# Optimization experiments

Measured on AMD Instinct MI355X. Metric: run time of the kernel, lower is better.

Reference implementation:

```python
import jax, jax.numpy as jnp
import numpy as np

N_NODES, N_EDGES, F_IN, H1, H2, N_CLASSES = 10000, 640000, 128, 64, 32, 16


def gcn_conv(x, W, b, src, dst, n_nodes):
    """PyG GCNConv: x' = D^{-1/2} (A + I) D^{-1/2} (x W) + b, deg from dst + self-loop."""
    h = x @ W  # [N, out]
    deg = jax.ops.segment_sum(jnp.ones(src.shape[0], h.dtype), dst,
                              num_segments=n_nodes) + 1.0  # +1 self-loop
    dinv = jax.lax.rsqrt(deg)  # [N]
    coef = dinv[src] * dinv[dst]  # [E]
    agg = jax.ops.segment_sum(h[src] * coef[:, None], dst, num_segments=n_nodes)
    agg = agg + h * (dinv * dinv)[:, None]  # self-loop contribution
    return agg + b


def setup_inputs() -> dict:
    key = jax.random.key(0)
    ks = jax.random.split(key, 8)
    x = jax.random.normal(ks[0], (N_NODES, F_IN), jnp.float32)
    edge_index = jax.random.randint(ks[1], (2, N_EDGES), 0, N_NODES, jnp.int32)
    W1 = jax.random.normal(ks[2], (F_IN, H1), jnp.float32) / np.sqrt(F_IN)
    b1 = jnp.zeros((H1,), jnp.float32)
    W2 = jax.random.normal(ks[3], (H1, H2), jnp.float32) / np.sqrt(H1)
    b2 = jnp.zeros((H2,), jnp.float32)
    Wfc = jax.random.normal(ks[4], (H2, N_CLASSES), jnp.float32) / np.sqrt(H2)
    bfc = jnp.zeros((N_CLASSES,), jnp.float32)
    return {"x": x, "W1": W1, "b1": b1, "W2": W2, "b2": b2,
            "Wfc": Wfc, "bfc": bfc, "edge_index": edge_index}


def reference(x, W1, b1, W2, b2, Wfc, bfc, edge_index):
    src, dst = edge_index[0], edge_index[1]
    n = x.shape[0]
    h = jax.nn.relu(gcn_conv(x, W1, b1, src, dst, n))
    # dropout p=0.5 is identity in eval mode
    h = jax.nn.relu(gcn_conv(h, W2, b2, src, dst, n))
    g = jnp.mean(h, axis=0)  # [H2]
    return g @ Wfc + bfc  # [num_classes]
```

## Files before the change

kernel.cpp:

```cpp
#include <hip/hip_runtime.h>
#include <hip/hip_bf16.h>

#define N_NODES 10000
#define N_EDGES 640000
#define F_IN 128
#define H1 64
#define H2 32
#define N_CLASSES 16

#define NB 128
#define NPB 79
#define STAGE_C 64
#define SLOT 6144
#define IDX_CAP 4096
#define PART_BLOCKS 313

typedef unsigned short ushortT;

__device__ __forceinline__ float bf_lo(unsigned u) {
    u <<= 16; float f; __builtin_memcpy(&f, &u, 4); return f;
}
__device__ __forceinline__ float bf_hi(unsigned u) {
    u &= 0xffff0000u; float f; __builtin_memcpy(&f, &u, 4); return f;
}
__device__ __forceinline__ unsigned bf_pack(float a, float b) {
    __hip_bfloat16 ha = __float2bfloat16(a), hb = __float2bfloat16(b);
    unsigned short ua, ub;
    __builtin_memcpy(&ua, &ha, 2); __builtin_memcpy(&ub, &hb, 2);
    return (unsigned)ua | ((unsigned)ub << 16);
}

__global__ void __launch_bounds__(256) k_part_gemm1(const int* __restrict__ src,
                                                    const int* __restrict__ dst,
                                                    int* __restrict__ bucketCursor,
                                                    int* __restrict__ partBuf,
                                                    const float* __restrict__ x,
                                                    const float* __restrict__ W1,
                                                    float* __restrict__ h1f,
                                                    const float* __restrict__ bfc,
                                                    float* __restrict__ out) {
    __shared__ __align__(16) char pool[40960];
    int t = threadIdx.x;
    if (blockIdx.x < PART_BLOCKS) {
        int* cnt   = (int*)pool;
        int* gbase = (int*)(pool + 512);
        int* stage = (int*)(pool + 1024);
        if (t < NB) cnt[t] = 0;
        __syncthreads();
        const int4* src4 = (const int4*)src;
        const int4* dst4 = (const int4*)dst;
#pragma unroll
        for (int k = 0; k < 2; ++k) {
            int i4 = blockIdx.x * 512 + k * 256 + t;
            if (i4 < N_EDGES / 4) {
                int4 s = src4[i4];
                int4 d = dst4[i4];
                int b, l, p;
                b = d.x / NPB; l = d.x - b * NPB; p = atomicAdd(&cnt[b], 1); stage[b * STAGE_C + p] = s.x | (l << 14);
                b = d.y / NPB; l = d.y - b * NPB; p = atomicAdd(&cnt[b], 1); stage[b * STAGE_C + p] = s.y | (l << 14);
                b = d.z / NPB; l = d.z - b * NPB; p = atomicAdd(&cnt[b], 1); stage[b * STAGE_C + p] = s.z | (l << 14);
                b = d.w / NPB; l = d.w - b * NPB; p = atomicAdd(&cnt[b], 1); stage[b * STAGE_C + p] = s.w | (l << 14);
            }
        }
        __syncthreads();
        if (t < NB) gbase[t] = atomicAdd(&bucketCursor[t], cnt[t]);
        __syncthreads();
        for (int i = t; i < NB * STAGE_C; i += 256) {
            int b = i >> 6;
            int k = i & (STAGE_C - 1);
            if (k < cnt[b]) partBuf[b * SLOT + gbase[b] + k] = stage[i];
        }
    } else {
        int gb = blockIdx.x - PART_BLOCKS;
        float* w1s = (float*)pool;
        float* xs  = (float*)(pool + 32768);
        int node0 = gb * 16;
        const float4* W14 = (const float4*)W1;
        float4* w1s4 = (float4*)w1s;
#pragma unroll
        for (int i = 0; i < 8; ++i) w1s4[i * 256 + t] = W14[i * 256 + t];
        const float4* x4 = (const float4*)(x + (long)node0 * F_IN);
        float4* xs4 = (float4*)xs;
#pragma unroll
        for (int i = 0; i < 2; ++i) xs4[i * 256 + t] = x4[i * 256 + t];
        if (gb == 0 && t < N_CLASSES) out[t] = bfc[t];
        __syncthreads();
        int j = t & 63;
        int q = t >> 6;
        int r0 = q * 4;
        float acc0 = 0.f, acc1 = 0.f, acc2 = 0.f, acc3 = 0.f;
#pragma unroll 4
        for (int k = 0; k < F_IN; ++k) {
            float w = w1s[k * H1 + j];
            acc0 += xs[(r0 + 0) * F_IN + k] * w;
            acc1 += xs[(r0 + 1) * F_IN + k] * w;
            acc2 += xs[(r0 + 2) * F_IN + k] * w;
            acc3 += xs[(r0 + 3) * F_IN + k] * w;
        }
        int v0 = node0 + r0;
        h1f[(v0 + 0) * H1 + j] = acc0;
        h1f[(v0 + 1) * H1 + j] = acc1;
        h1f[(v0 + 2) * H1 + j] = acc2;
        h1f[(v0 + 3) * H1 + j] = acc3;
    }
}

__global__ void __launch_bounds__(512) k_bsort(const int* __restrict__ bucketCursor,
                                               const int* __restrict__ partBuf,
                                               ushortT* __restrict__ srcU,
                                               int* __restrict__ rowStart,
                                               float* __restrict__ dinv,
                                               const float* __restrict__ h1f,
                                               __hip_bfloat16* __restrict__ h1b) {
    __shared__ int sc[NB];
    __shared__ int ldeg[NPB];
    __shared__ int lpre[NPB];
    __shared__ int cur[NPB];
    __shared__ float sdv[NPB];
    int t = threadIdx.x;
    int b = blockIdx.x;
    if (b == 0 && t == 0) rowStart[N_NODES] = N_EDGES;
    if (t < NB) sc[t] = bucketCursor[t];
    __syncthreads();
    for (int off = 1; off < NB; off <<= 1) {
        int v = (t >= off && t < NB) ? sc[t - off] : 0;
        __syncthreads();
        if (t < NB) sc[t] += v;
        __syncthreads();
    }
    int cnt = bucketCursor[b];
    int base = sc[b] - cnt;
    int nodeBase = b * NPB;
    int nNodes = N_NODES - nodeBase;
    if (nNodes <= 0) return;
    if (nNodes > NPB) nNodes = NPB;
    if (t < NPB) ldeg[t] = 0;
    __syncthreads();
    for (int i = t; i < cnt; i += 512) {
        int p = partBuf[b * SLOT + i];
        atomicAdd(&ldeg[p >> 14], 1);
    }
    __syncthreads();
    if (t == 0) {
        int run = 0;
        for (int i = 0; i < nNodes; ++i) { lpre[i] = run; run += ldeg[i]; }
    }
    __syncthreads();
    if (t < nNodes) {
        int v = nodeBase + t;
        rowStart[v] = base + lpre[t];
        cur[t] = lpre[t];
        float dv_ = rsqrtf((float)ldeg[t] + 1.0f);
        dinv[v] = dv_;
        sdv[t] = dv_;
    }
    __syncthreads();
    for (int i = t; i < cnt; i += 512) {
        int p = partBuf[b * SLOT + i];
        int pos = atomicAdd(&cur[p >> 14], 1);
        srcU[base + pos] = (ushortT)(p & 16383);
    }
    unsigned* h1u = (unsigned*)h1b;
    for (int i = t; i < nNodes * 32; i += 512) {
        int ln = i >> 5, p = i & 31;
        int v = nodeBase + ln;
        float2 f2 = ((const float2*)(h1f + v * H1))[p];
        float d = sdv[ln];
        h1u[v * 32 + p] = bf_pack(f2.x * d, f2.y * d);
    }
}

__global__ void __launch_bounds__(256) k_gather1_gemm2(const __hip_bfloat16* __restrict__ h1b,
                                const int* __restrict__ rowStart,
                                const ushortT* __restrict__ srcU,
                                const float* __restrict__ dinv,
                                const float* __restrict__ b1,
                                const float* __restrict__ W2,
                                __hip_bfloat16* __restrict__ h2b) {
    __shared__ float h1s[8][H1];
    __shared__ ushortT idxs[IDX_CAP];
    __shared__ int sRange[2];
    int t = threadIdx.x;
    int n  = t >> 5;
    int fp = t & 31;
    int v = blockIdx.x * 8 + n;
    if (t == 0) { sRange[0] = rowStart[blockIdx.x * 8]; sRange[1] = rowStart[blockIdx.x * 8 + 8]; }
    __syncthreads();
    int rs0 = sRange[0];
    int cnt0 = sRange[1] - rs0;
    bool useLds = (cnt0 <= IDX_CAP);
    if (useLds) for (int i = t; i < cnt0; i += 256) idxs[i] = srcU[rs0 + i];
    float dv_ = dinv[v];
    int rs = rowStart[v], re = rowStart[v + 1];
    const unsigned* h1u = (const unsigned*)h1b;
    unsigned su = h1u[v * 32 + fp];
    float fx = bf_lo(su), fy = bf_hi(su);
    float x0 = 0.f, y0 = 0.f, x1 = 0.f, y1 = 0.f;
    float x2 = 0.f, y2 = 0.f, x3 = 0.f, y3 = 0.f;
    __syncthreads();
    if (useLds) {
        int le = rs - rs0, lend = re - rs0;
        for (; le + 4 <= lend; le += 4) {
            int i0 = idxs[le],     i1 = idxs[le + 1];
            int i2 = idxs[le + 2], i3 = idxs[le + 3];
            unsigned u0 = h1u[i0 * 32 + fp];
            unsigned u1 = h1u[i1 * 32 + fp];
            unsigned u2 = h1u[i2 * 32 + fp];
            unsigned u3 = h1u[i3 * 32 + fp];
            x0 += bf_lo(u0); y0 += bf_hi(u0);
            x1 += bf_lo(u1); y1 += bf_hi(u1);
            x2 += bf_lo(u2); y2 += bf_hi(u2);
            x3 += bf_lo(u3); y3 += bf_hi(u3);
        }
        for (; le < lend; ++le) {
            unsigned u = h1u[idxs[le] * 32 + fp];
            fx += bf_lo(u); fy += bf_hi(u);
        }
    } else {
        for (int e = rs; e < re; ++e) {
            unsigned u = h1u[(int)srcU[e] * 32 + fp];
            fx += bf_lo(u); fy += bf_hi(u);
        }
    }
    fx += (x0 + x1) + (x2 + x3);
    fy += (y0 + y1) + (y2 + y3);
    ((float2*)h1s[n])[fp] = make_float2(fmaxf(dv_ * fx + b1[fp * 2], 0.f),
                                        fmaxf(dv_ * fy + b1[fp * 2 + 1], 0.f));
    __syncthreads();
    float acc = 0.f;
#pragma unroll
    for (int kk = 0; kk < H1; ++kk)
        acc += h1s[n][kk] * W2[kk * H2 + fp];
    h2b[v * H2 + fp] = __float2bfloat16(acc * dv_);
}

__global__ void __launch_bounds__(256) k_gather2_out(const __hip_bfloat16* __restrict__ h2b,
                               const int* __restrict__ rowStart,
                               const ushortT* __restrict__ srcU,
                               const float* __restrict__ dinv,
                               const float* __restrict__ b2,
                               const float* __restrict__ Wfc,
                               float* __restrict__ out) {
    __shared__ float red[16][H2];
    __shared__ ushortT idxs[IDX_CAP];
    __shared__ int sRange[2];
    __shared__ float gs[H2];
    int t = threadIdx.x;
    int n  = t >> 4;
    int fp = t & 15;
    int v = blockIdx.x * 16 + n;
    if (t == 0) { sRange[0] = rowStart[blockIdx.x * 16]; sRange[1] = rowStart[blockIdx.x * 16 + 16]; }
    __syncthreads();
    int rs0 = sRange[0];
    int cnt0 = sRange[1] - rs0;
    bool useLds = (cnt0 <= IDX_CAP);
    if (useLds) for (int i = t; i < cnt0; i += 256) idxs[i] = srcU[rs0 + i];
    float dv_ = dinv[v];
    int rs = rowStart[v], re = rowStart[v + 1];
    const unsigned* h2u = (const unsigned*)h2b;
    unsigned su = h2u[v * 16 + fp];
    float fx = bf_lo(su), fy = bf_hi(su);
    float x0 = 0.f, y0 = 0.f, x1 = 0.f, y1 = 0.f;
    float x2 = 0.f, y2 = 0.f, x3 = 0.f, y3 = 0.f;
    __syncthreads();
    if (useLds) {
        int le = rs - rs0, lend = re - rs0;
        for (; le + 4 <= lend; le += 4) {
            int i0 = idxs[le],     i1 = idxs[le + 1];
            int i2 = idxs[le + 2], i3 = idxs[le + 3];
            unsigned u0 = h2u[i0 * 16 + fp];
            unsigned u1 = h2u[i1 * 16 + fp];
            unsigned u2 = h2u[i2 * 16 + fp];
            unsigned u3 = h2u[i3 * 16 + fp];
            x0 += bf_lo(u0); y0 += bf_hi(u0);
            x1 += bf_lo(u1); y1 += bf_hi(u1);
            x2 += bf_lo(u2); y2 += bf_hi(u2);
            x3 += bf_lo(u3); y3 += bf_hi(u3);
        }
        for (; le < lend; ++le) {
            unsigned u = h2u[idxs[le] * 16 + fp];
            fx += bf_lo(u); fy += bf_hi(u);
        }
    } else {
        for (int e = rs; e < re; ++e) {
            unsigned u = h2u[(int)srcU[e] * 16 + fp];
            fx += bf_lo(u); fy += bf_hi(u);
        }
    }
    fx += (x0 + x1) + (x2 + x3);
    fy += (y0 + y1) + (y2 + y3);
    ((float2*)red[n])[fp] = make_float2(fmaxf(dv_ * fx + b2[fp * 2], 0.f),
                                        fmaxf(dv_ * fy + b2[fp * 2 + 1], 0.f));
    __syncthreads();
    if (t < H2) {
        float s = 0.f;
#pragma unroll
        for (int r = 0; r < 16; ++r) s += red[r][t];
        gs[t] = s;
    }
    __syncthreads();
    if (t < N_CLASSES) {
        float acc = 0.f;
#pragma unroll
        for (int j = 0; j < H2; ++j)
            acc += gs[j] * Wfc[j * N_CLASSES + t];
        atomicAdd(&out[t], acc * (1.0f / (float)N_NODES));
    }
}

extern "C" void kernel_launch(void* const* d_in, const int* in_sizes, int n_in,
                              void* d_out, int out_size, void* d_ws, size_t ws_size,
                              hipStream_t stream) {
    const float* x   = (const float*)d_in[0];
    const float* W1  = (const float*)d_in[1];
    const float* b1  = (const float*)d_in[2];
    const float* W2  = (const float*)d_in[3];
    const float* b2  = (const float*)d_in[4];
    const float* Wfc = (const float*)d_in[5];
    const float* bfc = (const float*)d_in[6];
    const int* edge = (const int*)d_in[7];
    const int* srcI = edge;
    const int* dstI = edge + N_EDGES;
    float* out = (float*)d_out;

    char* ws = (char*)d_ws;
    int*     bucketCursor = (int*)    (ws + 0);
    float*   dinv         = (float*)  (ws + 1024);
    int*     rowStart     = (int*)    (ws + 41984);
    ushortT* srcU         = (ushortT*)(ws + 82944);
    int*     partBuf      = (int*)    (ws + 1363968);
    float*   h1f          = (float*)  (ws + 4509696);
    __hip_bfloat16* h1b   = (__hip_bfloat16*)(ws + 7069696);
    __hip_bfloat16* h2b   = (__hip_bfloat16*)(ws + 8349696);

    hipMemsetAsync(bucketCursor, 0, 512, stream);

    k_part_gemm1<<<PART_BLOCKS + N_NODES / 16, 256, 0, stream>>>(
        srcI, dstI, bucketCursor, partBuf, x, W1, h1f, bfc, out);
    k_bsort<<<NB, 512, 0, stream>>>(bucketCursor, partBuf, srcU, rowStart, dinv,
                                    h1f, h1b);
    k_gather1_gemm2<<<N_NODES / 8, 256, 0, stream>>>(h1b, rowStart, srcU,
                                                     dinv, b1, W2, h2b);
    k_gather2_out<<<N_NODES / 16, 256, 0, stream>>>(h2b, rowStart, srcU,
                                                    dinv, b2, Wfc, out);
}
```

Before: 125.9 us.

## Replace global bucket atomics with per-block counts and fixed-slot CSR layout

Partition blocks now write their staged edges and per-bucket counts to fixed per-block slots instead of reserving space through global atomics, so the memset and the global atomic cursor go away. The sort kernel gathers each bucket's pieces from all partition blocks into LDS and places each bucket's CSR at a fixed offset, so rowEnd is needed and the prefix scan across buckets disappears. GEMM1 now writes bf16 h1 directly, which removes the fp32 intermediate buffer. The cost is a larger, sparser partBuf that the sort kernel must scan (313×64 slots per bucket), plus some bf16 double rounding of h1.

```diff
diff --git a/kernel.cpp b/kernel.cpp
--- a/kernel.cpp
+++ b/kernel.cpp
@@ -9,6 +9,7 @@
 #define N_CLASSES 16
 
 #define NB 128
+#define NUSED 127
 #define NPB 79
 #define STAGE_C 64
 #define SLOT 6144
@@ -32,19 +33,18 @@
 
 __global__ void __launch_bounds__(256) k_part_gemm1(const int* __restrict__ src,
                                                     const int* __restrict__ dst,
-                                                    int* __restrict__ bucketCursor,
+                                                    ushortT* __restrict__ blockCnt,
                                                     int* __restrict__ partBuf,
                                                     const float* __restrict__ x,
                                                     const float* __restrict__ W1,
-                                                    float* __restrict__ h1f,
+                                                    __hip_bfloat16* __restrict__ h1b,
                                                     const float* __restrict__ bfc,
                                                     float* __restrict__ out) {
     __shared__ __align__(16) char pool[40960];
     int t = threadIdx.x;
     if (blockIdx.x < PART_BLOCKS) {
         int* cnt   = (int*)pool;
-        int* gbase = (int*)(pool + 512);
-        int* stage = (int*)(pool + 1024);
+        int* stage = (int*)(pool + 512);
         if (t < NB) cnt[t] = 0;
         __syncthreads();
         const int4* src4 = (const int4*)src;
@@ -63,12 +63,11 @@
             }
         }
         __syncthreads();
-        if (t < NB) gbase[t] = atomicAdd(&bucketCursor[t], cnt[t]);
-        __syncthreads();
+        if (t < NB) blockCnt[blockIdx.x * NB + t] = (ushortT)cnt[t];
         for (int i = t; i < NB * STAGE_C; i += 256) {
             int b = i >> 6;
             int k = i & (STAGE_C - 1);
-            if (k < cnt[b]) partBuf[b * SLOT + gbase[b] + k] = stage[i];
+            if (k < cnt[b]) partBuf[blockIdx.x * (NB * STAGE_C) + i] = stage[i];
         }
     } else {
         int gb = blockIdx.x - PART_BLOCKS;
@@ -98,65 +97,65 @@
             acc3 += xs[(r0 + 3) * F_IN + k] * w;
         }
         int v0 = node0 + r0;
-        h1f[(v0 + 0) * H1 + j] = acc0;
-        h1f[(v0 + 1) * H1 + j] = acc1;
-        h1f[(v0 + 2) * H1 + j] = acc2;
-        h1f[(v0 + 3) * H1 + j] = acc3;
-    }
-}
-
-__global__ void __launch_bounds__(512) k_bsort(const int* __restrict__ bucketCursor,
+        h1b[(v0 + 0) * H1 + j] = __float2bfloat16(acc0);
+        h1b[(v0 + 1) * H1 + j] = __float2bfloat16(acc1);
+        h1b[(v0 + 2) * H1 + j] = __float2bfloat16(acc2);
+        h1b[(v0 + 3) * H1 + j] = __float2bfloat16(acc3);
+    }
+}
+
+__global__ void __launch_bounds__(512) k_bsort(const ushortT* __restrict__ blockCnt,
                                                const int* __restrict__ partBuf,
                                                ushortT* __restrict__ srcU,
                                                int* __restrict__ rowStart,
+                                               int* __restrict__ rowEnd,
                                                float* __restrict__ dinv,
-                                               const float* __restrict__ h1f,
                                                __hip_bfloat16* __restrict__ h1b) {
-    __shared__ int sc[NB];
+    __shared__ ushortT cntL[PART_BLOCKS];
+    __shared__ int stageL[SLOT];
     __shared__ int ldeg[NPB];
     __shared__ int lpre[NPB];
     __shared__ int cur[NPB];
     __shared__ float sdv[NPB];
+    __shared__ int nStage;
     int t = threadIdx.x;
     int b = blockIdx.x;
-    if (b == 0 && t == 0) rowStart[N_NODES] = N_EDGES;
-    if (t < NB) sc[t] = bucketCursor[t];
-    __syncthreads();
-    for (int off = 1; off < NB; off <<= 1) {
-        int v = (t >= off && t < NB) ? sc[t - off] : 0;
-        __syncthreads();
-        if (t < NB) sc[t] += v;
-        __syncthreads();
-    }
-    int cnt = bucketCursor[b];
-    int base = sc[b] - cnt;
+    for (int i = t; i < PART_BLOCKS; i += 512) cntL[i] = blockCnt[i * NB + b];
+    if (t < NPB) ldeg[t] = 0;
+    if (t == 0) nStage = 0;
+    __syncthreads();
+    for (int i = t; i < PART_BLOCKS * STAGE_C; i += 512) {
+        int blk = i >> 6, k = i & (STAGE_C - 1);
+        if (k < (int)cntL[blk]) {
+            int p = partBuf[blk * (NB * STAGE_C) + b * STAGE_C + k];
+            int pos = atomicAdd(&nStage, 1);
+            stageL[pos] = p;
+            atomicAdd(&ldeg[p >> 14], 1);
+        }
+    }
+    __syncthreads();
     int nodeBase = b * NPB;
     int nNodes = N_NODES - nodeBase;
-    if (nNodes <= 0) return;
     if (nNodes > NPB) nNodes = NPB;
-    if (t < NPB) ldeg[t] = 0;
-    __syncthreads();
-    for (int i = t; i < cnt; i += 512) {
-        int p = partBuf[b * SLOT + i];
-        atomicAdd(&ldeg[p >> 14], 1);
-    }
-    __syncthreads();
     if (t == 0) {
         int run = 0;
         for (int i = 0; i < nNodes; ++i) { lpre[i] = run; run += ldeg[i]; }
     }
     __syncthreads();
+    int base = b * SLOT;
     if (t < nNodes) {
         int v = nodeBase + t;
         rowStart[v] = base + lpre[t];
+        rowEnd[v]   = base + lpre[t] + ldeg[t];
         cur[t] = lpre[t];
         float dv_ = rsqrtf((float)ldeg[t] + 1.0f);
         dinv[v] = dv_;
         sdv[t] = dv_;
     }
     __syncthreads();
-    for (int i = t; i < cnt; i += 512) {
-        int p = partBuf[b * SLOT + i];
+    int total = nStage;
+    for (int i = t; i < total; i += 512) {
+        int p = stageL[i];
         int pos = atomicAdd(&cur[p >> 14], 1);
         srcU[base + pos] = (ushortT)(p & 16383);
     }
@@ -164,14 +163,15 @@
     for (int i = t; i < nNodes * 32; i += 512) {
         int ln = i >> 5, p = i & 31;
         int v = nodeBase + ln;
-        float2 f2 = ((const float2*)(h1f + v * H1))[p];
+        unsigned u = h1u[v * 32 + p];
         float d = sdv[ln];
-        h1u[v * 32 + p] = bf_pack(f2.x * d, f2.y * d);
+        h1u[v * 32 + p] = bf_pack(bf_lo(u) * d, bf_hi(u) * d);
     }
 }
 
 __global__ void __launch_bounds__(256) k_gather1_gemm2(const __hip_bfloat16* __restrict__ h1b,
                                 const int* __restrict__ rowStart,
+                                const int* __restrict__ rowEnd,
                                 const ushortT* __restrict__ srcU,
                                 const float* __restrict__ dinv,
                                 const float* __restrict__ b1,
@@ -184,14 +184,14 @@
     int n  = t >> 5;
     int fp = t & 31;
     int v = blockIdx.x * 8 + n;
-    if (t == 0) { sRange[0] = rowStart[blockIdx.x * 8]; sRange[1] = rowStart[blockIdx.x * 8 + 8]; }
+    if (t == 0) { sRange[0] = rowStart[blockIdx.x * 8]; sRange[1] = rowEnd[blockIdx.x * 8 + 7]; }
     __syncthreads();
     int rs0 = sRange[0];
     int cnt0 = sRange[1] - rs0;
     bool useLds = (cnt0 <= IDX_CAP);
     if (useLds) for (int i = t; i < cnt0; i += 256) idxs[i] = srcU[rs0 + i];
     float dv_ = dinv[v];
-    int rs = rowStart[v], re = rowStart[v + 1];
+    int rs = rowStart[v], re = rowEnd[v];
     const unsigned* h1u = (const unsigned*)h1b;
     unsigned su = h1u[v * 32 + fp];
     float fx = bf_lo(su), fy = bf_hi(su);
@@ -236,6 +236,7 @@
 
 __global__ void __launch_bounds__(256) k_gather2_out(const __hip_bfloat16* __restrict__ h2b,
                                const int* __restrict__ rowStart,
+                               const int* __restrict__ rowEnd,
                                const ushortT* __restrict__ srcU,
                                const float* __restrict__ dinv,
                                const float* __restrict__ b2,
@@ -249,14 +250,14 @@
     int n  = t >> 4;
     int fp = t & 15;
     int v = blockIdx.x * 16 + n;
-    if (t == 0) { sRange[0] = rowStart[blockIdx.x * 16]; sRange[1] = rowStart[blockIdx.x * 16 + 16]; }
+    if (t == 0) { sRange[0] = rowStart[blockIdx.x * 16]; sRange[1] = rowEnd[blockIdx.x * 16 + 15]; }
     __syncthreads();
     int rs0 = sRange[0];
     int cnt0 = sRange[1] - rs0;
     bool useLds = (cnt0 <= IDX_CAP);
     if (useLds) for (int i = t; i < cnt0; i += 256) idxs[i] = srcU[rs0 + i];
     float dv_ = dinv[v];
-    int rs = rowStart[v], re = rowStart[v + 1];
+    int rs = rowStart[v], re = rowEnd[v];
     const unsigned* h2u = (const unsigned*)h2b;
     unsigned su = h2u[v * 16 + fp];
     float fx = bf_lo(su), fy = bf_hi(su);
@@ -324,23 +325,21 @@
     float* out = (float*)d_out;
 
     char* ws = (char*)d_ws;
-    int*     bucketCursor = (int*)    (ws + 0);
-    float*   dinv         = (float*)  (ws + 1024);
-    int*     rowStart     = (int*)    (ws + 41984);
-    ushortT* srcU         = (ushortT*)(ws + 82944);
-    int*     partBuf      = (int*)    (ws + 1363968);
-    float*   h1f          = (float*)  (ws + 4509696);
-    __hip_bfloat16* h1b   = (__hip_bfloat16*)(ws + 7069696);
-    __hip_bfloat16* h2b   = (__hip_bfloat16*)(ws + 8349696);
-
-    hipMemsetAsync(bucketCursor, 0, 512, stream);
+    ushortT* blockCnt = (ushortT*)(ws + 0);
+    int*     rowStart = (int*)    (ws + 81920);
+    int*     rowEnd   = (int*)    (ws + 122880);
+    float*   dinv     = (float*)  (ws + 163840);
+    ushortT* srcU     = (ushortT*)(ws + 204800);
+    int*     partBuf  = (int*)    (ws + 1765376);
+    __hip_bfloat16* h1b = (__hip_bfloat16*)(ws + 12021760);
+    __hip_bfloat16* h2b = (__hip_bfloat16*)(ws + 13301760);
 
     k_part_gemm1<<<PART_BLOCKS + N_NODES / 16, 256, 0, stream>>>(
-        srcI, dstI, bucketCursor, partBuf, x, W1, h1f, bfc, out);
-    k_bsort<<<NB, 512, 0, stream>>>(bucketCursor, partBuf, srcU, rowStart, dinv,
-                                    h1f, h1b);
-    k_gather1_gemm2<<<N_NODES / 8, 256, 0, stream>>>(h1b, rowStart, srcU,
+        srcI, dstI, blockCnt, partBuf, x, W1, h1b, bfc, out);
+    k_bsort<<<NUSED, 512, 0, stream>>>(blockCnt, partBuf, srcU, rowStart, rowEnd,
+                                       dinv, h1b);
+    k_gather1_gemm2<<<N_NODES / 8, 256, 0, stream>>>(h1b, rowStart, rowEnd, srcU,
                                                      dinv, b1, W2, h2b);
-    k_gather2_out<<<N_NODES / 16, 256, 0, stream>>>(h2b, rowStart, srcU,
+    k_gather2_out<<<N_NODES / 16, 256, 0, stream>>>(h2b, rowStart, rowEnd, srcU,
                                                     dinv, b2, Wfc, out);
 }
```

Measured after the change: 129.9 us. 3.1% more time.
